# Kernel optimization log

Hardware: AMD Instinct MI355X
Metric: run time of the kernel (lower is better)

The kernel has to match this reference:

```python
import jax, jax.numpy as jnp
import numpy as np

IN_CH, OUT_CH = 64, 32
V1, V2 = 40962, 163842  # icosahedral levels; V2 = 4*V1 - 6
B = 4
EPS = 1e-5
SLOPE = 0.2  # LeakyReLU negative slope


def setup_inputs() -> dict:
    key = jax.random.key(0)
    ks = jax.random.split(key, 8)
    return {
        "x1": jax.random.normal(ks[0], (B, IN_CH, V1), jnp.float32),
        "x2": jax.random.normal(ks[1], (B, OUT_CH, V2), jnp.float32),
        "neigh_orders": jax.random.randint(ks[2], (7 * V2,), 0, V2, jnp.int32),
        "upconv_top_index": jax.random.randint(ks[3], (V1,), 0, V1 * 7, jnp.int32),
        "upconv_down_index": jax.random.randint(ks[4], (2 * (V2 - V1),), 0, V1 * 7, jnp.int32),
        "W_up": jax.random.normal(ks[5], (7 * OUT_CH, IN_CH), jnp.float32) * 0.05,
        "b_up": jnp.zeros((7 * OUT_CH,), jnp.float32),
        "W1": jax.random.normal(ks[6], (OUT_CH, 7 * 2 * OUT_CH), jnp.float32) * 0.05,
        "b1": jnp.zeros((OUT_CH,), jnp.float32),
        "g1": jnp.ones((OUT_CH,), jnp.float32),
        "be1": jnp.zeros((OUT_CH,), jnp.float32),
        "W2": jax.random.normal(ks[7], (OUT_CH, 7 * OUT_CH), jnp.float32) * 0.05,
        "b2": jnp.zeros((OUT_CH,), jnp.float32),
        "g2": jnp.ones((OUT_CH,), jnp.float32),
        "be2": jnp.zeros((OUT_CH,), jnp.float32),
    }


def _bn_lrelu(x, g, b):
    # BatchNorm1d with track_running_stats=False: always uses current (per-sample) batch stats,
    # biased variance, over the vertex axis. Then LeakyReLU(0.2).
    mu = x.mean(axis=0)
    var = x.var(axis=0)  # biased (ddof=0), matches torch BN normalization
    y = (x - mu) * jax.lax.rsqrt(var + EPS) * g + b
    return jnp.where(y >= 0, y, SLOPE * y)


def _one_sample(x1b, x2b, neigh, top, down,
                W_up, b_up, W1, b1, g1, be1, W2, b2, g2, be2):
    # upconv: Linear(in_ch -> 7*out_ch), scatter to the finer mesh via index gathers
    raw = x1b.T @ W_up.T + b_up                      # (V1, 7*OUT_CH)
    flat = raw.reshape(V1 * 7, OUT_CH)
    y_top = flat[top]                                # (V1, OUT_CH)
    y_down = flat[down].reshape(-1, OUT_CH, 2).mean(axis=-1)  # (V2-V1, OUT_CH), torch view semantics
    y1 = jnp.concatenate([y_top, y_down], axis=0)    # (V2, OUT_CH)
    y = jnp.concatenate([y1, x2b.T], axis=1)         # (V2, 2*OUT_CH) skip-concat
    # one-ring conv 1: gather 7 neighbors, flatten, GEMM
    m = y[neigh].reshape(V2, 7 * 2 * OUT_CH)
    h = _bn_lrelu(m @ W1.T + b1, g1, be1)            # (V2, OUT_CH)
    # one-ring conv 2
    m2 = h[neigh].reshape(V2, 7 * OUT_CH)
    h2 = _bn_lrelu(m2 @ W2.T + b2, g2, be2)          # (V2, OUT_CH)
    return h2.T                                      # (OUT_CH, V2)


def reference(x1, x2, neigh_orders, upconv_top_index, upconv_down_index,
              W_up, b_up, W1, b1, g1, be1, W2, b2, g2, be2):
    f = lambda a, b: _one_sample(a, b, neigh_orders, upconv_top_index, upconv_down_index,
                                 W_up, b_up, W1, b1, g1, be1, W2, b2, g2, be2)
    return jax.vmap(f)(x1, x2)  # (B, OUT_CH, V2)
```

## Files before the change

### kernel.cpp

```cpp
#include <hip/hip_runtime.h>

#define V1n 40962
#define V2n 163842
#define Bn  4
#define T2S 163848

typedef _Float16 h8   __attribute__((ext_vector_type(8)));
typedef _Float16 h2   __attribute__((ext_vector_type(2)));
typedef float    f32x4 __attribute__((ext_vector_type(4)));

__device__ __forceinline__ float h2f(_Float16 h) { return (float)h; }

__global__ __launch_bounds__(256) void k_pack_up(const float* __restrict__ Wup,
                                                 _Float16* __restrict__ WupP) {
  int i = blockIdx.x * 256 + threadIdx.x;
  if (i >= 14336) return;
  int e = i & 7, col = (i >> 3) & 15, g = i >> 7;
  int nt = g % 14, kq = g / 14;
  int j = nt * 16 + col;
  int k = (kq >> 2) * 32 + (kq & 3) * 8 + e;
  WupP[i] = (_Float16)Wup[j * 64 + k];
}

__global__ __launch_bounds__(256, 4) void k_upconv(const float* __restrict__ x1,
    const float* __restrict__ bup, const _Float16* __restrict__ WupP,
    _Float16* __restrict__ rawq) {
  int lane = threadIdx.x & 63, wv = threadIdx.x >> 6;
  int col = lane & 15, quad = lane >> 4;
  int v0 = blockIdx.x * 16;
  int v = v0 + col;
  int vc = min(v, V1n - 1);
  const float* xb = x1 + ((size_t)wv * 64) * V1n + vc;
  h8 a0, a1;
#pragma unroll
  for (int e = 0; e < 8; ++e) a0[e] = (_Float16)xb[(size_t)(quad * 8 + e) * V1n];
#pragma unroll
  for (int e = 0; e < 8; ++e) a1[e] = (_Float16)xb[(size_t)(32 + quad * 8 + e) * V1n];
  f32x4 acc[14];
#pragma unroll
  for (int nt = 0; nt < 14; ++nt) {
    float bv = bup[nt * 16 + col];
    acc[nt] = (f32x4){bv, bv, bv, bv};
  }
  const _Float16* wp0 = WupP + (size_t)(quad * 14) * 128 + col * 8;
  const _Float16* wp1 = WupP + (size_t)((4 + quad) * 14) * 128 + col * 8;
#pragma unroll
  for (int nt = 0; nt < 14; ++nt) {
    h8 bb = *(const h8*)(wp0 + nt * 128);
    acc[nt] = __builtin_amdgcn_mfma_f32_16x16x32_f16(a0, bb, acc[nt], 0, 0, 0);
  }
#pragma unroll
  for (int nt = 0; nt < 14; ++nt) {
    h8 bb = *(const h8*)(wp1 + nt * 128);
    acc[nt] = __builtin_amdgcn_mfma_f32_16x16x32_f16(a1, bb, acc[nt], 0, 0, 0);
  }
  __shared__ _Float16 lds[16 * 912];
#pragma unroll
  for (int nt = 0; nt < 14; ++nt) {
    int gofs = (nt >> 1) * 128 + wv * 32 + (nt & 1) * 16 + col;
#pragma unroll
    for (int r = 0; r < 4; ++r)
      lds[(quad * 4 + r) * 912 + gofs] = (_Float16)acc[nt][r];
  }
  __syncthreads();
  int rem = V1n - v0;
  _Float16* dst = rawq + (size_t)v0 * 896;
#pragma unroll
  for (int i = 0; i < 7; ++i) {
    int m = i * 256 + (int)threadIdx.x;
    int vr = m / 112;
    int r1 = m - vr * 112;
    if (vr < rem)
      *(h8*)(dst + (size_t)m * 8) = *(const h8*)(lds + vr * 912 + r1 * 8);
  }
}

__global__ __launch_bounds__(256) void k_assemble(const float* __restrict__ x2,
    const int* __restrict__ top, const int* __restrict__ down,
    const _Float16* __restrict__ rawq, _Float16* __restrict__ y) {
  int t = blockIdx.x * 256 + threadIdx.x;
  int v = t >> 2, b = t & 3;
  if (v >= V2n) return;
  h8 r0, r1, r2, r3;
  if (v < V1n) {
    int f = top[v];
    const _Float16* src = rawq + ((size_t)f * 4 + b) * 32;
    r0 = *(const h8*)src;        r1 = *(const h8*)(src + 8);
    r2 = *(const h8*)(src + 16); r3 = *(const h8*)(src + 24);
  } else {
    int k = v - V1n;
    int d0 = down[2 * k], d1 = down[2 * k + 1];
    const _Float16* se = rawq + ((size_t)d0 * 4 + b) * 32;
    const _Float16* so = rawq + ((size_t)d1 * 4 + b) * 32;
    h8 a0 = *(const h8*)se,        a1 = *(const h8*)(se + 8);
    h8 a2 = *(const h8*)(se + 16), a3 = *(const h8*)(se + 24);
    h8 c0 = *(const h8*)so,        c1 = *(const h8*)(so + 8);
    h8 c2 = *(const h8*)(so + 16), c3 = *(const h8*)(so + 24);
#pragma unroll
    for (int i = 0; i < 4; ++i) {
      r0[i]     = (_Float16)(0.5f * (h2f(a0[2 * i]) + h2f(a0[2 * i + 1])));
      r0[4 + i] = (_Float16)(0.5f * (h2f(a1[2 * i]) + h2f(a1[2 * i + 1])));
      r1[i]     = (_Float16)(0.5f * (h2f(a2[2 * i]) + h2f(a2[2 * i + 1])));
      r1[4 + i] = (_Float16)(0.5f * (h2f(a3[2 * i]) + h2f(a3[2 * i + 1])));
      r2[i]     = (_Float16)(0.5f * (h2f(c0[2 * i]) + h2f(c0[2 * i + 1])));
      r2[4 + i] = (_Float16)(0.5f * (h2f(c1[2 * i]) + h2f(c1[2 * i + 1])));
      r3[i]     = (_Float16)(0.5f * (h2f(c2[2 * i]) + h2f(c2[2 * i + 1])));
      r3[4 + i] = (_Float16)(0.5f * (h2f(c3[2 * i]) + h2f(c3[2 * i + 1])));
    }
  }
  _Float16* dst = y + ((size_t)b * V2n + v) * 64;
  *(h8*)(dst)      = r0; *(h8*)(dst + 8)  = r1;
  *(h8*)(dst + 16) = r2; *(h8*)(dst + 24) = r3;
  const float* xp = x2 + (size_t)b * 32 * V2n + v;
#pragma unroll
  for (int g2 = 0; g2 < 4; ++g2) {
    h8 px;
#pragma unroll
    for (int e = 0; e < 8; ++e) px[e] = (_Float16)xp[(size_t)(g2 * 8 + e) * V2n];
    *(h8*)(dst + 32 + g2 * 8) = px;
  }
}

__global__ __launch_bounds__(256) void k_pack(const float* __restrict__ W1,
    const float* __restrict__ W2, _Float16* __restrict__ W1p,
    _Float16* __restrict__ W2p) {
  int i = blockIdx.x * 256 + threadIdx.x;
  if (i < 14336) {
    int e = i & 7, o = (i >> 3) & 31, g = i >> 8;
    int k = (g >> 2) * 32 + (g & 3) * 8 + e;
    W1p[i] = (_Float16)W1[o * 448 + k];
  }
  int i2 = i - 14336;
  if (i2 >= 0 && i2 < 7168) {
    int e = i2 & 7, o = (i2 >> 3) & 31, g = i2 >> 8;
    int k = (g >> 2) * 32 + (g & 3) * 8 + e;
    W2p[i2] = (_Float16)W2[o * 224 + k];
  }
}

__global__ __launch_bounds__(256, 4) void k_conv1(const _Float16* __restrict__ y,
    const int* __restrict__ neigh, const _Float16* __restrict__ W1p,
    _Float16* __restrict__ t1, float* __restrict__ sumsR) {
  int b = blockIdx.y;
  int lane = threadIdx.x & 63, wv = threadIdx.x >> 6;
  int col = lane & 15, quad = lane >> 4;
  int v0 = blockIdx.x * 64 + wv * 16;
  int v = v0 + col;
  int vc = min(v, V2n - 1);
  const int* np = neigh + 7 * (size_t)vc;
  int idx[7];
#pragma unroll
  for (int j = 0; j < 7; ++j) idx[j] = np[j];
  const _Float16* yb = y + (size_t)b * V2n * 64 + quad * 8;
  h8 a[14];
#pragma unroll
  for (int j = 0; j < 7; ++j) {
    const _Float16* r = yb + (size_t)idx[j] * 64;
    a[2 * j]     = *(const h8*)r;
    a[2 * j + 1] = *(const h8*)(r + 32);
  }
  f32x4 acc0 = {0.f, 0.f, 0.f, 0.f}, acc1 = {0.f, 0.f, 0.f, 0.f};
  const _Float16* wp = W1p + quad * 256;
#pragma unroll
  for (int kt = 0; kt < 14; ++kt) {
    h8 b0 = *(const h8*)(wp + (size_t)kt * 1024 + col * 8);
    h8 b1 = *(const h8*)(wp + (size_t)kt * 1024 + (16 + col) * 8);
    acc0 = __builtin_amdgcn_mfma_f32_16x16x32_f16(a[kt], b0, acc0, 0, 0, 0);
    acc1 = __builtin_amdgcn_mfma_f32_16x16x32_f16(a[kt], b1, acc1, 0, 0, 0);
  }
  __shared__ _Float16 tile[4][16][32];
  __shared__ float red[4][4][16];
#pragma unroll
  for (int r = 0; r < 4; ++r) {
    tile[wv][quad * 4 + r][col]      = (_Float16)acc0[r];
    tile[wv][quad * 4 + r][16 + col] = (_Float16)acc1[r];
  }
  __syncthreads();
  int row = threadIdx.x >> 2, ch = threadIdx.x & 3;
  int vv = blockIdx.x * 64 + row;
  float s[8], q[8];
#pragma unroll
  for (int e = 0; e < 8; ++e) { s[e] = 0.f; q[e] = 0.f; }
  if (vv < V2n) {
    h8 val = *(const h8*)&tile[row >> 4][row & 15][ch * 8];
    *(h8*)(t1 + ((size_t)vv * 4 + b) * 32 + ch * 8) = val;
#pragma unroll
    for (int e = 0; e < 8; ++e) { float x = h2f(val[e]); s[e] = x; q[e] = x * x; }
  }
#pragma unroll
  for (int m = 4; m <= 32; m <<= 1) {
#pragma unroll
    for (int e = 0; e < 8; ++e) { s[e] += __shfl_xor(s[e], m); q[e] += __shfl_xor(q[e], m); }
  }
  if (lane < 4) {
#pragma unroll
    for (int e = 0; e < 8; ++e) { red[wv][lane][e] = s[e]; red[wv][lane][8 + e] = q[e]; }
  }
  __syncthreads();
  if (threadIdx.x < 64) {
    int chh = threadIdx.x >> 4, e = threadIdx.x & 15;
    float v4 = red[0][chh][e] + red[1][chh][e] + red[2][chh][e] + red[3][chh][e];
    int c = chh * 8 + (e & 7);
    int rep = blockIdx.x & 63;
    float* dst = sumsR + rep * 256 + ((e < 8) ? (b * 32 + c) : (128 + b * 32 + c));
    atomicAdd(dst, v4);
  }
}

__global__ void k_finalize(const float* __restrict__ sumsR, const float* __restrict__ g,
                           const float* __restrict__ be, float* __restrict__ sc,
                           float* __restrict__ sh) {
  int i = threadIdx.x;
  if (i >= 128) return;
  float s = 0.f, q = 0.f;
  for (int r = 0; r < 64; ++r) { s += sumsR[r * 256 + i]; q += sumsR[r * 256 + 128 + i]; }
  float inv = 1.0f / (float)V2n;
  float mu = s * inv;
  float var = fmaf(q, inv, -mu * mu);
  float rs = rsqrtf(var + 1e-5f);
  int o = i & 31;
  float scale = rs * g[o];
  sc[i] = scale;
  sh[i] = fmaf(-mu, scale, be[o]);
}

__global__ __launch_bounds__(256, 3) void k_conv2(const _Float16* __restrict__ t1,
    const int* __restrict__ neigh, const _Float16* __restrict__ W2p,
    const float* __restrict__ sc1, const float* __restrict__ sh1,
    _Float16* __restrict__ t2, float* __restrict__ sumsR) {
  int lane = threadIdx.x & 63, wv = threadIdx.x >> 6;
  int col = lane & 15, quad = lane >> 4;
  int v0 = blockIdx.x * 64 + wv * 16;
  int v = v0 + col;
  int vc = min(v, V2n - 1);
  const int* np = neigh + 7 * (size_t)vc;
  int idx[7];
#pragma unroll
  for (int j = 0; j < 7; ++j) idx[j] = np[j];
  float sc[4][8], sh[4][8];
#pragma unroll
  for (int b = 0; b < 4; ++b)
#pragma unroll
    for (int i = 0; i < 8; ++i) {
      sc[b][i] = sc1[b * 32 + quad * 8 + i];
      sh[b][i] = sh1[b * 32 + quad * 8 + i];
    }
  f32x4 acc[4][2];
#pragma unroll
  for (int b = 0; b < 4; ++b) {
    acc[b][0] = (f32x4){0.f, 0.f, 0.f, 0.f};
    acc[b][1] = (f32x4){0.f, 0.f, 0.f, 0.f};
  }
  const _Float16* wp = W2p + quad * 256;
#pragma unroll
  for (int j = 0; j < 7; ++j) {
    const _Float16* r = t1 + (size_t)idx[j] * 128 + quad * 8;
    h8 raws[4];
#pragma unroll
    for (int b = 0; b < 4; ++b) raws[b] = *(const h8*)(r + b * 32);
    h8 w0 = *(const h8*)(wp + (size_t)j * 1024 + col * 8);
    h8 w1 = *(const h8*)(wp + (size_t)j * 1024 + (16 + col) * 8);
#pragma unroll
    for (int b = 0; b < 4; ++b) {
      h8 aa;
#pragma unroll
      for (int e = 0; e < 8; ++e) {
        float f = fmaf(h2f(raws[b][e]), sc[b][e], sh[b][e]);
        f = fmaxf(f, 0.2f * f);
        aa[e] = (_Float16)f;
      }
      acc[b][0] = __builtin_amdgcn_mfma_f32_16x16x32_f16(aa, w0, acc[b][0], 0, 0, 0);
      acc[b][1] = __builtin_amdgcn_mfma_f32_16x16x32_f16(aa, w1, acc[b][1], 0, 0, 0);
    }
  }
  __shared__ float red2[4][16][4];
  int vrow = v0 + quad * 4;
  bool tailblk = (blockIdx.x == gridDim.x - 1);
  int rep = blockIdx.x & 63;
#pragma unroll
  for (int b = 0; b < 4; ++b) {
    if (b) __syncthreads();
    float s0 = 0.f, q0 = 0.f, s1 = 0.f, q1 = 0.f;
    _Float16* tb = t2 + (size_t)b * 32 * T2S;
    if (!tailblk) {
      _Float16* p0 = tb + (size_t)col * T2S + vrow;
      _Float16* p1 = tb + (size_t)(16 + col) * T2S + vrow;
      *(h2*)(p0)     = (h2){(_Float16)acc[b][0][0], (_Float16)acc[b][0][1]};
      *(h2*)(p0 + 2) = (h2){(_Float16)acc[b][0][2], (_Float16)acc[b][0][3]};
      *(h2*)(p1)     = (h2){(_Float16)acc[b][1][0], (_Float16)acc[b][1][1]};
      *(h2*)(p1 + 2) = (h2){(_Float16)acc[b][1][2], (_Float16)acc[b][1][3]};
#pragma unroll
      for (int rr = 0; rr < 4; ++rr) {
        s0 += acc[b][0][rr]; q0 += acc[b][0][rr] * acc[b][0][rr];
        s1 += acc[b][1][rr]; q1 += acc[b][1][rr] * acc[b][1][rr];
      }
    } else {
#pragma unroll
      for (int rr = 0; rr < 4; ++rr) {
        if (vrow + rr < V2n) {
          tb[(size_t)col * T2S + vrow + rr]        = (_Float16)acc[b][0][rr];
          tb[(size_t)(16 + col) * T2S + vrow + rr] = (_Float16)acc[b][1][rr];
          s0 += acc[b][0][rr]; q0 += acc[b][0][rr] * acc[b][0][rr];
          s1 += acc[b][1][rr]; q1 += acc[b][1][rr] * acc[b][1][rr];
        }
      }
    }
#pragma unroll
    for (int m = 16; m <= 32; m <<= 1) {
      s0 += __shfl_xor(s0, m); q0 += __shfl_xor(q0, m);
      s1 += __shfl_xor(s1, m); q1 += __shfl_xor(q1, m);
    }
    if (lane < 16) {
      red2[wv][col][0] = s0; red2[wv][col][1] = q0;
      red2[wv][col][2] = s1; red2[wv][col][3] = q1;
    }
    __syncthreads();
    if (threadIdx.x < 64) {
      int cc = threadIdx.x & 15, which = threadIdx.x >> 4;
      float v4 = red2[0][cc][which] + red2[1][cc][which] +
                 red2[2][cc][which] + red2[3][cc][which];
      int c = (which & 2) ? cc + 16 : cc;
      float* dstp = sumsR + rep * 256 + ((which & 1) ? (128 + b * 32 + c) : (b * 32 + c));
      atomicAdd(dstp, v4);
    }
  }
}

__global__ __launch_bounds__(256) void k_bnorm(const _Float16* __restrict__ t2,
    const float* __restrict__ sc, const float* __restrict__ sh,
    float* __restrict__ out) {
  int row = blockIdx.y, qrt = blockIdx.x;
  float scale = sc[row], shift = sh[row];
  const _Float16* p = t2 + (size_t)row * T2S;
  float* o = out + (size_t)row * V2n;
  int c0 = qrt * 5120;
  for (int cch = c0 + (int)threadIdx.x; cch < c0 + 5120; cch += 256) {
    h8 x = *(const h8*)(p + (size_t)cch * 8);
    float* ob = o + (size_t)cch * 8;
    float f0, f1;
#pragma unroll
    for (int e = 0; e < 4; ++e) {
      f0 = fmaf((float)x[2 * e], scale, shift);     f0 = fmaxf(f0, 0.2f * f0);
      f1 = fmaf((float)x[2 * e + 1], scale, shift); f1 = fmaxf(f1, 0.2f * f1);
      *(float2*)(ob + 2 * e) = make_float2(f0, f1);
    }
  }
  if (qrt == 3 && threadIdx.x < 2) {
    int i = 163840 + (int)threadIdx.x;
    float a = fmaf((float)p[i], scale, shift);
    o[i] = fmaxf(a, 0.2f * a);
  }
}

extern "C" void kernel_launch(void* const* d_in, const int* in_sizes, int n_in,
                              void* d_out, int out_size, void* d_ws, size_t ws_size,
                              hipStream_t stream) {
  const float* x1   = (const float*)d_in[0];
  const float* x2   = (const float*)d_in[1];
  const int*   neigh= (const int*)d_in[2];
  const int*   top  = (const int*)d_in[3];
  const int*   down = (const int*)d_in[4];
  const float* Wup  = (const float*)d_in[5];
  const float* bup  = (const float*)d_in[6];
  const float* W1   = (const float*)d_in[7];
  const float* g1   = (const float*)d_in[9];
  const float* be1  = (const float*)d_in[10];
  const float* W2   = (const float*)d_in[11];
  const float* g2   = (const float*)d_in[13];
  const float* be2  = (const float*)d_in[14];
  float* out = (float*)d_out;

  char* ws = (char*)d_ws;
  _Float16* rawq = (_Float16*)ws;
  _Float16* y    = (_Float16*)(ws + 73403904);
  _Float16* t1   = (_Float16*)(ws + 157291008);
  float* stats   = (float*)(ws + 199234560);
  float* sc1 = stats;        float* sh1 = stats + 128;
  float* sc2 = stats + 256;  float* sh2 = stats + 384;
  _Float16* WupP = t1;
  _Float16* W1p  = rawq;
  _Float16* W2p  = rawq + 14336;
  float* sumsR1 = (float*)(ws + (1 << 20));
  float* sumsR2 = (float*)(ws + (1 << 20) + 65536);
  _Float16* t2  = (_Float16*)(ws + (2 << 20));

  k_pack_up  <<<56, 256, 0, stream>>>(Wup, WupP);
  k_upconv   <<<2561, 256, 0, stream>>>(x1, bup, WupP, rawq);
  k_assemble <<<2561, 256, 0, stream>>>(x2, top, down, rawq, y);
  k_pack     <<<84, 256, 0, stream>>>(W1, W2, W1p, W2p);
  hipMemsetAsync(sumsR1, 0, 131072, stream);
  k_conv1    <<<dim3(2561, Bn), 256, 0, stream>>>(y, neigh, W1p, t1, sumsR1);
  k_finalize <<<1, 128, 0, stream>>>(sumsR1, g1, be1, sc1, sh1);
  k_conv2    <<<2561, 256, 0, stream>>>(t1, neigh, W2p, sc1, sh1, t2, sumsR2);
  k_finalize <<<1, 128, 0, stream>>>(sumsR2, g2, be2, sc2, sh2);
  k_bnorm    <<<dim3(4, 128),   256, 0, stream>>>(t2, sc2, sh2, out);
}
```

Before: 460.4 us.

## Stage W1 in LDS and pipeline neighbor gathers with explicit waitcnt in conv1

Each block of conv1 now copies the packed W1 weights (28 KB) into shared memory, and the MFMA loop reads B operands from LDS instead of global/L2. The 14 neighbor-row gathers are issued as inline-asm global loads, and each MFMA step waits only on its own loads through decreasing vmcnt counts, so compute overlaps the outstanding gathers. Occupancy hint drops from 4 to 2 blocks per CU because of the larger LDS footprint. The inline asm depends on the compiler not inserting other vector memory ops between the loads, which would make the vmcnt counts wrong.

```diff
diff --git a/kernel.cpp b/kernel.cpp
--- a/kernel.cpp
+++ b/kernel.cpp
@@ -138,12 +138,18 @@
   }
 }
 
-__global__ __launch_bounds__(256, 4) void k_conv1(const _Float16* __restrict__ y,
+__global__ __launch_bounds__(256, 2) void k_conv1(const _Float16* __restrict__ y,
     const int* __restrict__ neigh, const _Float16* __restrict__ W1p,
     _Float16* __restrict__ t1, float* __restrict__ sumsR) {
+  __shared__ _Float16 w1s[14336];
+  __shared__ _Float16 tile[4][16][32];
+  __shared__ float red[4][4][16];
   int b = blockIdx.y;
   int lane = threadIdx.x & 63, wv = threadIdx.x >> 6;
   int col = lane & 15, quad = lane >> 4;
+#pragma unroll
+  for (int i = 0; i < 7; ++i)
+    ((h8*)w1s)[i * 256 + (int)threadIdx.x] = ((const h8*)W1p)[i * 256 + (int)threadIdx.x];
   int v0 = blockIdx.x * 64 + wv * 16;
   int v = v0 + col;
   int vc = min(v, V2n - 1);
@@ -151,25 +157,32 @@
   int idx[7];
 #pragma unroll
   for (int j = 0; j < 7; ++j) idx[j] = np[j];
+  __syncthreads();
   const _Float16* yb = y + (size_t)b * V2n * 64 + quad * 8;
-  h8 a[14];
-#pragma unroll
-  for (int j = 0; j < 7; ++j) {
-    const _Float16* r = yb + (size_t)idx[j] * 64;
-    a[2 * j]     = *(const h8*)r;
-    a[2 * j + 1] = *(const h8*)(r + 32);
-  }
+  h8 a0_0, a1_0, a0_1, a1_1, a0_2, a1_2, a0_3, a1_3, a0_4, a1_4, a0_5, a1_5, a0_6, a1_6;
+#define GLD(J, A0v, A1v) { const _Float16* rp = yb + (size_t)idx[J] * 64;            \
+  asm volatile("global_load_dwordx4 %0, %2, off\n\t"                                 \
+               "global_load_dwordx4 %1, %2, off offset:64"                           \
+               : "=&v"(A0v), "=&v"(A1v) : "v"(rp)); }
+  GLD(0, a0_0, a1_0) GLD(1, a0_1, a1_1) GLD(2, a0_2, a1_2) GLD(3, a0_3, a1_3)
+  GLD(4, a0_4, a1_4) GLD(5, a0_5, a1_5) GLD(6, a0_6, a1_6)
+#undef GLD
   f32x4 acc0 = {0.f, 0.f, 0.f, 0.f}, acc1 = {0.f, 0.f, 0.f, 0.f};
-  const _Float16* wp = W1p + quad * 256;
-#pragma unroll
-  for (int kt = 0; kt < 14; ++kt) {
-    h8 b0 = *(const h8*)(wp + (size_t)kt * 1024 + col * 8);
-    h8 b1 = *(const h8*)(wp + (size_t)kt * 1024 + (16 + col) * 8);
-    acc0 = __builtin_amdgcn_mfma_f32_16x16x32_f16(a[kt], b0, acc0, 0, 0, 0);
-    acc1 = __builtin_amdgcn_mfma_f32_16x16x32_f16(a[kt], b1, acc1, 0, 0, 0);
-  }
-  __shared__ _Float16 tile[4][16][32];
-  __shared__ float red[4][4][16];
+  const _Float16* wq = w1s + quad * 256 + col * 8;
+#define STEP(J, CNT, A0v, A1v) {                                                     \
+  asm volatile("s_waitcnt vmcnt(" CNT ")" : "+v"(A0v), "+v"(A1v));                   \
+  h8 b00 = *(const h8*)(wq + (2 * J) * 1024);                                        \
+  h8 b01 = *(const h8*)(wq + (2 * J) * 1024 + 128);                                  \
+  acc0 = __builtin_amdgcn_mfma_f32_16x16x32_f16(A0v, b00, acc0, 0, 0, 0);            \
+  acc1 = __builtin_amdgcn_mfma_f32_16x16x32_f16(A0v, b01, acc1, 0, 0, 0);            \
+  h8 b10 = *(const h8*)(wq + (2 * J + 1) * 1024);                                    \
+  h8 b11 = *(const h8*)(wq + (2 * J + 1) * 1024 + 128);                              \
+  acc0 = __builtin_amdgcn_mfma_f32_16x16x32_f16(A1v, b10, acc0, 0, 0, 0);            \
+  acc1 = __builtin_amdgcn_mfma_f32_16x16x32_f16(A1v, b11, acc1, 0, 0, 0); }
+  STEP(0, "12", a0_0, a1_0) STEP(1, "10", a0_1, a1_1) STEP(2, "8", a0_2, a1_2)
+  STEP(3, "6",  a0_3, a1_3) STEP(4, "4",  a0_4, a1_4) STEP(5, "2", a0_5, a1_5)
+  STEP(6, "0",  a0_6, a1_6)
+#undef STEP
 #pragma unroll
   for (int r = 0; r < 4; ++r) {
     tile[wv][quad * 4 + r][col]      = (_Float16)acc0[r];
```

Measured after the change: 447.8 us. 1.03x faster.

## Stage weights in LDS and software-pipeline neighbor gathers in one-ring convs

Applied to the files above, without the earlier changes.

Conv1 now handles 128 vertices per block (two 16-vertex tiles per wave), with weights staged in LDS under a new MFMA-friendly pack layout. Tile B's gathers are issued through inline asm while tile A's MFMAs run, with explicit vmcnt waits. Conv2 is restructured so each wave handles one batch sample for 16 vertices, with more, smaller blocks and direct atomics instead of the LDS reduction. A sched_barrier is also added in assemble. The hand-managed vmcnt counts are fragile against compiler-inserted memory ops, and the larger LDS use may limit occupancy.

```diff
diff --git a/kernel.cpp b/kernel.cpp
--- a/kernel.cpp
+++ b/kernel.cpp
@@ -96,6 +96,7 @@
     h8 a2 = *(const h8*)(se + 16), a3 = *(const h8*)(se + 24);
     h8 c0 = *(const h8*)so,        c1 = *(const h8*)(so + 8);
     h8 c2 = *(const h8*)(so + 16), c3 = *(const h8*)(so + 24);
+    __builtin_amdgcn_sched_barrier(0);
 #pragma unroll
     for (int i = 0; i < 4; ++i) {
       r0[i]     = (_Float16)(0.5f * (h2f(a0[2 * i]) + h2f(a0[2 * i + 1])));
@@ -126,66 +127,105 @@
     _Float16* __restrict__ W2p) {
   int i = blockIdx.x * 256 + threadIdx.x;
   if (i < 14336) {
-    int e = i & 7, o = (i >> 3) & 31, g = i >> 8;
-    int k = (g >> 2) * 32 + (g & 3) * 8 + e;
-    W1p[i] = (_Float16)W1[o * 448 + k];
+    int e = i & 7, quad = (i >> 3) & 3, col = (i >> 5) & 15, half = (i >> 9) & 1, kt = i >> 10;
+    int o = half * 16 + col;
+    W1p[i] = (_Float16)W1[o * 448 + kt * 32 + quad * 8 + e];
   }
   int i2 = i - 14336;
   if (i2 >= 0 && i2 < 7168) {
-    int e = i2 & 7, o = (i2 >> 3) & 31, g = i2 >> 8;
-    int k = (g >> 2) * 32 + (g & 3) * 8 + e;
-    W2p[i2] = (_Float16)W2[o * 224 + k];
+    int e = i2 & 7, quad = (i2 >> 3) & 3, col = (i2 >> 5) & 15, half = (i2 >> 9) & 1, j = i2 >> 10;
+    int o = half * 16 + col;
+    W2p[i2] = (_Float16)W2[o * 224 + j * 32 + quad * 8 + e];
   }
 }
 
 __global__ __launch_bounds__(256, 4) void k_conv1(const _Float16* __restrict__ y,
     const int* __restrict__ neigh, const _Float16* __restrict__ W1p,
     _Float16* __restrict__ t1, float* __restrict__ sumsR) {
+  __shared__ _Float16 w1s[14336];
+  __shared__ _Float16 tile[8][16][32];
+  __shared__ float red[4][4][16];
   int b = blockIdx.y;
-  int lane = threadIdx.x & 63, wv = threadIdx.x >> 6;
+  int tid = threadIdx.x;
+  int lane = tid & 63, wv = tid >> 6;
   int col = lane & 15, quad = lane >> 4;
-  int v0 = blockIdx.x * 64 + wv * 16;
-  int v = v0 + col;
-  int vc = min(v, V2n - 1);
-  const int* np = neigh + 7 * (size_t)vc;
-  int idx[7];
-#pragma unroll
-  for (int j = 0; j < 7; ++j) idx[j] = np[j];
+#pragma unroll
+  for (int i = 0; i < 7; ++i)
+    ((h8*)w1s)[i * 256 + tid] = ((const h8*)W1p)[i * 256 + tid];
+  int v0 = blockIdx.x * 128 + wv * 32;
+  int vA = v0 + col, vB = v0 + 16 + col;
+  int vcA = min(vA, V2n - 1), vcB = min(vB, V2n - 1);
+  const int* npA = neigh + 7 * (size_t)vcA;
+  const int* npB = neigh + 7 * (size_t)vcB;
+  int idxA[7], idxB[7];
+#pragma unroll
+  for (int j = 0; j < 7; ++j) { idxA[j] = npA[j]; idxB[j] = npB[j]; }
+  __syncthreads();
   const _Float16* yb = y + (size_t)b * V2n * 64 + quad * 8;
-  h8 a[14];
-#pragma unroll
-  for (int j = 0; j < 7; ++j) {
-    const _Float16* r = yb + (size_t)idx[j] * 64;
-    a[2 * j]     = *(const h8*)r;
-    a[2 * j + 1] = *(const h8*)(r + 32);
-  }
-  f32x4 acc0 = {0.f, 0.f, 0.f, 0.f}, acc1 = {0.f, 0.f, 0.f, 0.f};
-  const _Float16* wp = W1p + quad * 256;
-#pragma unroll
-  for (int kt = 0; kt < 14; ++kt) {
-    h8 b0 = *(const h8*)(wp + (size_t)kt * 1024 + col * 8);
-    h8 b1 = *(const h8*)(wp + (size_t)kt * 1024 + (16 + col) * 8);
-    acc0 = __builtin_amdgcn_mfma_f32_16x16x32_f16(a[kt], b0, acc0, 0, 0, 0);
-    acc1 = __builtin_amdgcn_mfma_f32_16x16x32_f16(a[kt], b1, acc1, 0, 0, 0);
-  }
-  __shared__ _Float16 tile[4][16][32];
-  __shared__ float red[4][4][16];
+  h8 P0, P1, P2, P3, P4, P5, P6, P7, P8, P9, P10, P11, P12, P13;
+#define GA(J, RA, RB) { const _Float16* rp = yb + (size_t)idxA[J] * 64;              \
+  asm volatile("global_load_dwordx4 %0, %2, off\n\t"                                 \
+               "global_load_dwordx4 %1, %2, off offset:64"                           \
+               : "=&v"(RA), "=&v"(RB) : "v"(rp)); }
+  GA(0, P0, P1) GA(1, P2, P3) GA(2, P4, P5) GA(3, P6, P7)
+  GA(4, P8, P9) GA(5, P10, P11) GA(6, P12, P13)
+#undef GA
+  f32x4 accA0 = {0.f, 0.f, 0.f, 0.f}, accA1 = {0.f, 0.f, 0.f, 0.f};
+  const _Float16* wq = w1s + col * 32 + quad * 8;
+#define STEPA(J, RA, RB) {                                                           \
+  asm volatile("s_waitcnt vmcnt(12)" : "+v"(RA), "+v"(RB));                          \
+  h8 b00 = *(const h8*)(wq + (2 * J) * 1024);                                        \
+  h8 b01 = *(const h8*)(wq + (2 * J) * 1024 + 512);                                  \
+  accA0 = __builtin_amdgcn_mfma_f32_16x16x32_f16(RA, b00, accA0, 0, 0, 0);           \
+  accA1 = __builtin_amdgcn_mfma_f32_16x16x32_f16(RA, b01, accA1, 0, 0, 0);           \
+  h8 b10 = *(const h8*)(wq + (2 * J) * 1024 + 1024);                                 \
+  h8 b11 = *(const h8*)(wq + (2 * J) * 1024 + 1536);                                 \
+  accA0 = __builtin_amdgcn_mfma_f32_16x16x32_f16(RB, b10, accA0, 0, 0, 0);           \
+  accA1 = __builtin_amdgcn_mfma_f32_16x16x32_f16(RB, b11, accA1, 0, 0, 0);           \
+  const _Float16* rp = yb + (size_t)idxB[J] * 64;                                    \
+  asm volatile("global_load_dwordx4 %0, %2, off\n\t"                                 \
+               "global_load_dwordx4 %1, %2, off offset:64"                           \
+               : "=&v"(RA), "=&v"(RB) : "v"(rp)); }
+  STEPA(0, P0, P1) STEPA(1, P2, P3) STEPA(2, P4, P5) STEPA(3, P6, P7)
+  STEPA(4, P8, P9) STEPA(5, P10, P11) STEPA(6, P12, P13)
+#undef STEPA
+  f32x4 accB0 = {0.f, 0.f, 0.f, 0.f}, accB1 = {0.f, 0.f, 0.f, 0.f};
+#define STEPB(J, CNT, RA, RB) {                                                      \
+  asm volatile("s_waitcnt vmcnt(" CNT ")" : "+v"(RA), "+v"(RB));                     \
+  h8 b00 = *(const h8*)(wq + (2 * J) * 1024);                                        \
+  h8 b01 = *(const h8*)(wq + (2 * J) * 1024 + 512);                                  \
+  accB0 = __builtin_amdgcn_mfma_f32_16x16x32_f16(RA, b00, accB0, 0, 0, 0);           \
+  accB1 = __builtin_amdgcn_mfma_f32_16x16x32_f16(RA, b01, accB1, 0, 0, 0);           \
+  h8 b10 = *(const h8*)(wq + (2 * J) * 1024 + 1024);                                 \
+  h8 b11 = *(const h8*)(wq + (2 * J) * 1024 + 1536);                                 \
+  accB0 = __builtin_amdgcn_mfma_f32_16x16x32_f16(RB, b10, accB0, 0, 0, 0);           \
+  accB1 = __builtin_amdgcn_mfma_f32_16x16x32_f16(RB, b11, accB1, 0, 0, 0); }
+  STEPB(0, "12", P0, P1) STEPB(1, "10", P2, P3) STEPB(2, "8", P4, P5)
+  STEPB(3, "6",  P6, P7) STEPB(4, "4",  P8, P9) STEPB(5, "2", P10, P11)
+  STEPB(6, "0",  P12, P13)
+#undef STEPB
 #pragma unroll
   for (int r = 0; r < 4; ++r) {
-    tile[wv][quad * 4 + r][col]      = (_Float16)acc0[r];
-    tile[wv][quad * 4 + r][16 + col] = (_Float16)acc1[r];
+    tile[wv * 2][quad * 4 + r][col]          = (_Float16)accA0[r];
+    tile[wv * 2][quad * 4 + r][16 + col]     = (_Float16)accA1[r];
+    tile[wv * 2 + 1][quad * 4 + r][col]      = (_Float16)accB0[r];
+    tile[wv * 2 + 1][quad * 4 + r][16 + col] = (_Float16)accB1[r];
   }
   __syncthreads();
-  int row = threadIdx.x >> 2, ch = threadIdx.x & 3;
-  int vv = blockIdx.x * 64 + row;
+  int row = tid >> 2, ch = tid & 3;
   float s[8], q[8];
 #pragma unroll
   for (int e = 0; e < 8; ++e) { s[e] = 0.f; q[e] = 0.f; }
-  if (vv < V2n) {
-    h8 val = *(const h8*)&tile[row >> 4][row & 15][ch * 8];
-    *(h8*)(t1 + ((size_t)vv * 4 + b) * 32 + ch * 8) = val;
-#pragma unroll
-    for (int e = 0; e < 8; ++e) { float x = h2f(val[e]); s[e] = x; q[e] = x * x; }
+#pragma unroll
+  for (int h = 0; h < 2; ++h) {
+    int r128 = h * 64 + row;
+    int vv = blockIdx.x * 128 + r128;
+    if (vv < V2n) {
+      h8 val = *(const h8*)&tile[r128 >> 4][r128 & 15][ch * 8];
+      *(h8*)(t1 + ((size_t)vv * 4 + b) * 32 + ch * 8) = val;
+#pragma unroll
+      for (int e = 0; e < 8; ++e) { float x = h2f(val[e]); s[e] += x; q[e] += x * x; }
+    }
   }
 #pragma unroll
   for (int m = 4; m <= 32; m <<= 1) {
@@ -197,8 +237,8 @@
     for (int e = 0; e < 8; ++e) { red[wv][lane][e] = s[e]; red[wv][lane][8 + e] = q[e]; }
   }
   __syncthreads();
-  if (threadIdx.x < 64) {
-    int chh = threadIdx.x >> 4, e = threadIdx.x & 15;
+  if (tid < 64) {
+    int chh = tid >> 4, e = tid & 15;
     float v4 = red[0][chh][e] + red[1][chh][e] + red[2][chh][e] + red[3][chh][e];
     int c = chh * 8 + (e & 7);
     int rep = blockIdx.x & 63;
@@ -224,105 +264,91 @@
   sh[i] = fmaf(-mu, scale, be[o]);
 }
 
-__global__ __launch_bounds__(256, 3) void k_conv2(const _Float16* __restrict__ t1,
+__global__ __launch_bounds__(256, 4) void k_conv2(const _Float16* __restrict__ t1,
     const int* __restrict__ neigh, const _Float16* __restrict__ W2p,
     const float* __restrict__ sc1, const float* __restrict__ sh1,
     _Float16* __restrict__ t2, float* __restrict__ sumsR) {
-  int lane = threadIdx.x & 63, wv = threadIdx.x >> 6;
+  __shared__ _Float16 w2s[7168];
+  int tid = threadIdx.x;
+  int lane = tid & 63, b = tid >> 6;
   int col = lane & 15, quad = lane >> 4;
-  int v0 = blockIdx.x * 64 + wv * 16;
-  int v = v0 + col;
-  int vc = min(v, V2n - 1);
+  for (int i = tid; i < 896; i += 256)
+    ((h8*)w2s)[i] = ((const h8*)W2p)[i];
+  int v0 = blockIdx.x * 16;
+  int v = v0 + col, vc = min(v, V2n - 1);
   const int* np = neigh + 7 * (size_t)vc;
-  int idx[7];
-#pragma unroll
-  for (int j = 0; j < 7; ++j) idx[j] = np[j];
-  float sc[4][8], sh[4][8];
-#pragma unroll
-  for (int b = 0; b < 4; ++b)
-#pragma unroll
-    for (int i = 0; i < 8; ++i) {
-      sc[b][i] = sc1[b * 32 + quad * 8 + i];
-      sh[b][i] = sh1[b * 32 + quad * 8 + i];
+  int idx0 = np[0], idx1 = np[1], idx2 = np[2], idx3 = np[3],
+      idx4 = np[4], idx5 = np[5], idx6 = np[6];
+  float sc_[8], sh_[8];
+#pragma unroll
+  for (int i = 0; i < 8; ++i) {
+    sc_[i] = sc1[b * 32 + quad * 8 + i];
+    sh_[i] = sh1[b * 32 + quad * 8 + i];
+  }
+  __syncthreads();
+  const _Float16* t1b = t1 + b * 32 + quad * 8;
+  h8 P0, P1, P2, P3, P4, P5, P6;
+#define G2(IDX, R) { const _Float16* rp = t1b + (size_t)(IDX) * 128;                 \
+  asm volatile("global_load_dwordx4 %0, %1, off" : "=&v"(R) : "v"(rp)); }
+  G2(idx0, P0) G2(idx1, P1) G2(idx2, P2) G2(idx3, P3)
+  G2(idx4, P4) G2(idx5, P5) G2(idx6, P6)
+#undef G2
+  f32x4 acc0 = {0.f, 0.f, 0.f, 0.f}, acc1 = {0.f, 0.f, 0.f, 0.f};
+  const _Float16* wq = w2s + col * 32 + quad * 8;
+#define S2(J, CNT, R) {                                                              \
+  asm volatile("s_waitcnt vmcnt(" CNT ")" : "+v"(R));                                \
+  h8 aa;                                                                             \
+  _Pragma("unroll")                                                                  \
+  for (int e = 0; e < 8; ++e) {                                                      \
+    float f = fmaf(h2f(R[e]), sc_[e], sh_[e]);                                       \
+    f = fmaxf(f, 0.2f * f);                                                          \
+    aa[e] = (_Float16)f;                                                             \
+  }                                                                                  \
+  h8 w0 = *(const h8*)(wq + J * 1024);                                               \
+  h8 w1 = *(const h8*)(wq + J * 1024 + 512);                                         \
+  acc0 = __builtin_amdgcn_mfma_f32_16x16x32_f16(aa, w0, acc0, 0, 0, 0);              \
+  acc1 = __builtin_amdgcn_mfma_f32_16x16x32_f16(aa, w1, acc1, 0, 0, 0); }
+  S2(0, "6", P0) S2(1, "5", P1) S2(2, "4", P2) S2(3, "3", P3)
+  S2(4, "2", P4) S2(5, "1", P5) S2(6, "0", P6)
+#undef S2
+  int vrow = v0 + quad * 4;
+  float s0 = 0.f, q0 = 0.f, s1 = 0.f, q1 = 0.f;
+  _Float16* tb = t2 + (size_t)b * 32 * T2S;
+  if (blockIdx.x != gridDim.x - 1) {
+    _Float16* p0 = tb + (size_t)col * T2S + vrow;
+    _Float16* p1 = tb + (size_t)(16 + col) * T2S + vrow;
+    *(h2*)(p0)     = (h2){(_Float16)acc0[0], (_Float16)acc0[1]};
+    *(h2*)(p0 + 2) = (h2){(_Float16)acc0[2], (_Float16)acc0[3]};
+    *(h2*)(p1)     = (h2){(_Float16)acc1[0], (_Float16)acc1[1]};
+    *(h2*)(p1 + 2) = (h2){(_Float16)acc1[2], (_Float16)acc1[3]};
+#pragma unroll
+    for (int rr = 0; rr < 4; ++rr) {
+      s0 += acc0[rr]; q0 += acc0[rr] * acc0[rr];
+      s1 += acc1[rr]; q1 += acc1[rr] * acc1[rr];
     }
-  f32x4 acc[4][2];
-#pragma unroll
-  for (int b = 0; b < 4; ++b) {
-    acc[b][0] = (f32x4){0.f, 0.f, 0.f, 0.f};
-    acc[b][1] = (f32x4){0.f, 0.f, 0.f, 0.f};
-  }
-  const _Float16* wp = W2p + quad * 256;
-#pragma unroll
-  for (int j = 0; j < 7; ++j) {
-    const _Float16* r = t1 + (size_t)idx[j] * 128 + quad * 8;
-    h8 raws[4];
-#pragma unroll
-    for (int b = 0; b < 4; ++b) raws[b] = *(const h8*)(r + b * 32);
-    h8 w0 = *(const h8*)(wp + (size_t)j * 1024 + col * 8);
-    h8 w1 = *(const h8*)(wp + (size_t)j * 1024 + (16 + col) * 8);
-#pragma unroll
-    for (int b = 0; b < 4; ++b) {
-      h8 aa;
-#pragma unroll
-      for (int e = 0; e < 8; ++e) {
-        float f = fmaf(h2f(raws[b][e]), sc[b][e], sh[b][e]);
-        f = fmaxf(f, 0.2f * f);
-        aa[e] = (_Float16)f;
-      }
-      acc[b][0] = __builtin_amdgcn_mfma_f32_16x16x32_f16(aa, w0, acc[b][0], 0, 0, 0);
-      acc[b][1] = __builtin_amdgcn_mfma_f32_16x16x32_f16(aa, w1, acc[b][1], 0, 0, 0);
-    }
-  }
-  __shared__ float red2[4][16][4];
-  int vrow = v0 + quad * 4;
-  bool tailblk = (blockIdx.x == gridDim.x - 1);
-  int rep = blockIdx.x & 63;
-#pragma unroll
-  for (int b = 0; b < 4; ++b) {
-    if (b) __syncthreads();
-    float s0 = 0.f, q0 = 0.f, s1 = 0.f, q1 = 0.f;
-    _Float16* tb = t2 + (size_t)b * 32 * T2S;
-    if (!tailblk) {
-      _Float16* p0 = tb + (size_t)col * T2S + vrow;
-      _Float16* p1 = tb + (size_t)(16 + col) * T2S + vrow;
-      *(h2*)(p0)     = (h2){(_Float16)acc[b][0][0], (_Float16)acc[b][0][1]};
-      *(h2*)(p0 + 2) = (h2){(_Float16)acc[b][0][2], (_Float16)acc[b][0][3]};
-      *(h2*)(p1)     = (h2){(_Float16)acc[b][1][0], (_Float16)acc[b][1][1]};
-      *(h2*)(p1 + 2) = (h2){(_Float16)acc[b][1][2], (_Float16)acc[b][1][3]};
-#pragma unroll
-      for (int rr = 0; rr < 4; ++rr) {
-        s0 += acc[b][0][rr]; q0 += acc[b][0][rr] * acc[b][0][rr];
-        s1 += acc[b][1][rr]; q1 += acc[b][1][rr] * acc[b][1][rr];
-      }
-    } else {
-#pragma unroll
-      for (int rr = 0; rr < 4; ++rr) {
-        if (vrow + rr < V2n) {
-          tb[(size_t)col * T2S + vrow + rr]        = (_Float16)acc[b][0][rr];
-          tb[(size_t)(16 + col) * T2S + vrow + rr] = (_Float16)acc[b][1][rr];
-          s0 += acc[b][0][rr]; q0 += acc[b][0][rr] * acc[b][0][rr];
-          s1 += acc[b][1][rr]; q1 += acc[b][1][rr] * acc[b][1][rr];
-        }
+  } else {
+#pragma unroll
+    for (int rr = 0; rr < 4; ++rr) {
+      if (vrow + rr < V2n) {
+        tb[(size_t)col * T2S + vrow + rr]        = (_Float16)acc0[rr];
+        tb[(size_t)(16 + col) * T2S + vrow + rr] = (_Float16)acc1[rr];
+        s0 += acc0[rr]; q0 += acc0[rr] * acc0[rr];
+        s1 += acc1[rr]; q1 += acc1[rr] * acc1[rr];
       }
     }
-#pragma unroll
-    for (int m = 16; m <= 32; m <<= 1) {
-      s0 += __shfl_xor(s0, m); q0 += __shfl_xor(q0, m);
-      s1 += __shfl_xor(s1, m); q1 += __shfl_xor(q1, m);
-    }
-    if (lane < 16) {
-      red2[wv][col][0] = s0; red2[wv][col][1] = q0;
-      red2[wv][col][2] = s1; red2[wv][col][3] = q1;
-    }
-    __syncthreads();
-    if (threadIdx.x < 64) {
-      int cc = threadIdx.x & 15, which = threadIdx.x >> 4;
-      float v4 = red2[0][cc][which] + red2[1][cc][which] +
-                 red2[2][cc][which] + red2[3][cc][which];
-      int c = (which & 2) ? cc + 16 : cc;
-      float* dstp = sumsR + rep * 256 + ((which & 1) ? (128 + b * 32 + c) : (b * 32 + c));
-      atomicAdd(dstp, v4);
-    }
+  }
+#pragma unroll
+  for (int m = 16; m <= 32; m <<= 1) {
+    s0 += __shfl_xor(s0, m); q0 += __shfl_xor(q0, m);
+    s1 += __shfl_xor(s1, m); q1 += __shfl_xor(q1, m);
+  }
+  if (lane < 16) {
+    int rep = blockIdx.x & 63;
+    float* base = sumsR + rep * 256;
+    atomicAdd(base + b * 32 + col, s0);
+    atomicAdd(base + b * 32 + 16 + col, s1);
+    atomicAdd(base + 128 + b * 32 + col, q0);
+    atomicAdd(base + 128 + b * 32 + 16 + col, q1);
   }
 }
 
@@ -389,9 +415,9 @@
   k_assemble <<<2561, 256, 0, stream>>>(x2, top, down, rawq, y);
   k_pack     <<<84, 256, 0, stream>>>(W1, W2, W1p, W2p);
   hipMemsetAsync(sumsR1, 0, 131072, stream);
-  k_conv1    <<<dim3(2561, Bn), 256, 0, stream>>>(y, neigh, W1p, t1, sumsR1);
+  k_conv1    <<<dim3(1281, Bn), 256, 0, stream>>>(y, neigh, W1p, t1, sumsR1);
   k_finalize <<<1, 128, 0, stream>>>(sumsR1, g1, be1, sc1, sh1);
-  k_conv2    <<<2561, 256, 0, stream>>>(t1, neigh, W2p, sc1, sh1, t2, sumsR2);
+  k_conv2    <<<10241, 256, 0, stream>>>(t1, neigh, W2p, sc1, sh1, t2, sumsR2);
   k_finalize <<<1, 128, 0, stream>>>(sumsR2, g2, be2, sc2, sh2);
   k_bnorm    <<<dim3(4, 128),   256, 0, stream>>>(t2, sc2, sh2, out);
 }
```

Measured after the change: 445.6 us. -3.2%, faster.
